# Kernel optimization log

Measured on AMD Instinct MI355X. Metric: run time of the kernel, lower is better.

## Reference

```python
import jax, jax.numpy as jnp
import numpy as np

ODIM = 8192      # output dim (slice target)
MSIZE = 64       # tile size
N_BLOCKS = 1024  # size of shared block bank


def setup_inputs() -> dict:
    key = jax.random.key(0)
    k1, k2, k3, k4 = jax.random.split(key, 4)
    x = jax.random.normal(k1, (256, 8192), dtype=jnp.float32)
    # bank of msize x msize module blocks (scaled like fan-in init)
    blocks = jax.random.normal(k2, (N_BLOCKS, MSIZE, MSIZE), dtype=jnp.float32) * 0.02
    bound = 1.0 / np.sqrt(ODIM).astype(np.float32)
    bias = jax.random.uniform(k3, (ODIM,), dtype=jnp.float32, minval=-bound, maxval=bound)
    # parts: [icount, ocount] indices into the block bank
    parts = jax.random.randint(k4, (128, 128), 0, N_BLOCKS)
    return {"x": x, "blocks": blocks, "bias": bias, "parts": parts}


def reference(x, blocks, bias, parts):
    icount, ocount = parts.shape
    m = blocks.shape[-1]
    # build_mosaic: gather blocks per parts and tile into a dense weight matrix
    fc = blocks[parts]                                   # [ic, oc, m, m]
    fc_mat = fc.transpose(0, 2, 1, 3).reshape(icount * m, ocount * m)
    # idim (8192) is divisible by msize, so pad is identity (rem == 0 branch)
    y = x @ fc_mat                                       # [B, oc*m]
    y = y[..., :ODIM] + bias                             # slice + bias; post = Identity
    return y
```

## Files before the change

kernel.cpp:

```cpp
#include <hip/hip_runtime.h>
#include <stdint.h>

#define BATCH 256
#define IDIM  8192
#define ODIM  8192
#define MS    64
#define IC    128
#define OC    128
#define NB    1024

#define BM 256
#define BN 256
#define BK 64
#define KSPLIT 8
#define KT (IC / KSPLIT)

#define ABUF(s) ((s) * 16384)
#define BBUF(s) (32768 + (s) * 16384)

typedef __bf16 bf16x8 __attribute__((ext_vector_type(8)));
typedef float  floatx4 __attribute__((ext_vector_type(4)));

#define WAITCNT_VM(n) ((((n) & 15) | (((n) >> 4) << 14)) | 0x70 | 0xF00)

__device__ __forceinline__ void async_load16(unsigned short* lds_p, const unsigned short* g_p) {
    __builtin_amdgcn_global_load_lds(
        (const __attribute__((address_space(1))) unsigned int*)g_p,
        (__attribute__((address_space(3))) unsigned int*)lds_p,
        16, 0, 0);
}

__device__ __forceinline__ unsigned short f32_to_bf16(float f) {
    unsigned int u = __float_as_uint(f);
    u += 0x7FFFu + ((u >> 16) & 1u);
    return (unsigned short)(u >> 16);
}

#define XCONV_BLKS 1024
#define PT_BLKS 64
__global__ void k_convert(const float* __restrict__ x, const float* __restrict__ blocks,
                          const int* __restrict__ parts,
                          unsigned short* __restrict__ xb, unsigned short* __restrict__ bt,
                          int* __restrict__ pT) {
    __shared__ float tile[MS][MS + 1];
    int b = blockIdx.x;
    if (b < NB) {
        const float4* src4 = (const float4*)(blocks + (size_t)b * MS * MS);
        unsigned short* dst = bt + (size_t)b * MS * MS;
        #pragma unroll
        for (int i = 0; i < 4; ++i) {
            int slot = i * 256 + threadIdx.x;
            int r = slot >> 4, c4 = (slot & 15) * 4;
            float4 v = src4[slot];
            tile[r][c4 + 0] = v.x; tile[r][c4 + 1] = v.y;
            tile[r][c4 + 2] = v.z; tile[r][c4 + 3] = v.w;
        }
        __syncthreads();
        #pragma unroll
        for (int i = 0; i < 2; ++i) {
            int slot = i * 256 + threadIdx.x;
            int c = slot >> 3, o = slot & 7;
            union { unsigned short s[8]; uint4 v; } u;
            #pragma unroll
            for (int j = 0; j < 8; ++j) u.s[j] = f32_to_bf16(tile[o * 8 + j][c]);
            *(uint4*)(dst + c * MS + o * 8) = u.v;
        }
    } else if (b < NB + XCONV_BLKS) {
        int t = (b - NB) * 256 + threadIdx.x;
        const float4* x4 = (const float4*)x;
        float4 a = x4[2 * t], bb = x4[2 * t + 1];
        union { unsigned short s[8]; uint4 v; } u;
        u.s[0] = f32_to_bf16(a.x);  u.s[1] = f32_to_bf16(a.y);
        u.s[2] = f32_to_bf16(a.z);  u.s[3] = f32_to_bf16(a.w);
        u.s[4] = f32_to_bf16(bb.x); u.s[5] = f32_to_bf16(bb.y);
        u.s[6] = f32_to_bf16(bb.z); u.s[7] = f32_to_bf16(bb.w);
        ((uint4*)xb)[t] = u.v;
    } else {
        int t = (b - NB - XCONV_BLKS) * 256 + threadIdx.x;
        int oc = t >> 7, ic = t & 127;
        pT[t] = parts[ic * OC + oc];
    }
}

extern __shared__ unsigned short smem[];

__global__ __launch_bounds__(512, 2)
void k_mosaic_gemm(const unsigned short* __restrict__ xb,
                   const unsigned short* __restrict__ bt,
                   const int* __restrict__ pT,
                   float* __restrict__ partial) {
    const int tid  = threadIdx.x;
    const int lane = tid & 63;
    const int wave = tid >> 6;
    const int wrow = wave >> 2;
    const int wcol = wave & 3;
    const int ks = blockIdx.x;
    const int nt = blockIdx.y;

    const int ob0 = nt * 4;
    const int kb0 = ks * KT;

    const int row  = lane & 15;
    const int quad = lane >> 4;

    int pv = pT[(ob0 + quad) * IC + kb0 + row];

    const int swz0 = ((quad)     ^ (row & 7)) << 3;
    const int swz1 = ((quad + 4) ^ (row & 7)) << 3;
    const int a_b0 = (wrow * 128 + row) * MS + swz0;
    const int a_b1 = (wrow * 128 + row) * MS + swz1;
    const int b_b0 = (wcol * 64 + row) * MS + swz0;
    const int b_b1 = (wcol * 64 + row) * MS + swz1;

    floatx4 acc[8][4];
    #pragma unroll
    for (int mi = 0; mi < 8; ++mi)
        #pragma unroll
        for (int ni = 0; ni < 4; ++ni)
            acc[mi][ni] = (floatx4){0.f, 0.f, 0.f, 0.f};

    bf16x8 af[4], bfr[4];

#define STAGE_A(dstS, kb) do {                                                \
    _Pragma("unroll")                                                         \
    for (int j = 0; j < 4; ++j) {                                             \
        int slot = j * 512 + tid;               \
        int m = slot >> 3;                                                    \
        int oct = (slot & 7) ^ (m & 7);                                       \
        async_load16(smem + ABUF(dstS) + slot * 8,                            \
                     xb + (size_t)m * IDIM + (kb) * MS + oct * 8);            \
    } } while (0)

#define STAGE_B(dstS, t) do {                                                 \
    _Pragma("unroll")                                                         \
    for (int j = 0; j < 4; ++j) {                                             \
        int q = __shfl(pv, j * 16 + (t));                                     \
        int slot = j * 512 + tid;                                             \
        int n = slot >> 3;                                                    \
        int oct = (slot & 7) ^ (n & 7);                                       \
        async_load16(smem + BBUF(dstS) + slot * 8,                            \
                     bt + (size_t)q * (MS * MS) + (n & 63) * MS + oct * 8);   \
    } } while (0)

#define BARRIER_PIN() do {                                                    \
    __builtin_amdgcn_sched_barrier(0);                                        \
    __builtin_amdgcn_s_barrier();                                             \
    __builtin_amdgcn_sched_barrier(0); } while (0)

#define LOAD_A(S, abase, mh) do {                                             \
    _Pragma("unroll")                                                         \
    for (int mi = 0; mi < 4; ++mi)                                            \
        af[mi] = *(const bf16x8*)(smem + ABUF(S) + (abase) + (mh) * 4096 + mi * 1024); \
    } while (0)

#define LOAD_B(S, bbase) do {                                                 \
    _Pragma("unroll")                                                         \
    for (int ni = 0; ni < 4; ++ni)                                            \
        bfr[ni] = *(const bf16x8*)(smem + BBUF(S) + (bbase) + ni * 1024);     \
    } while (0)

#define MFMA16(mh) do {                                                       \
    __builtin_amdgcn_s_setprio(1);                                            \
    _Pragma("unroll")                                                         \
    for (int mi = 0; mi < 4; ++mi)                                            \
        _Pragma("unroll")                                                     \
        for (int ni = 0; ni < 4; ++ni)                                        \
            acc[(mh) * 4 + mi][ni] = __builtin_amdgcn_mfma_f32_16x16x32_bf16( \
                af[mi], bfr[ni], acc[(mh) * 4 + mi][ni], 0, 0, 0);            \
    __builtin_amdgcn_s_setprio(0); } while (0)

#define TILE(t, curS, nxtS, DO_STAGE) do {                                    \
                                         \
    LOAD_A(curS, a_b0, 0); LOAD_B(curS, b_b0);                                \
    if (DO_STAGE) STAGE_A(nxtS, kb0 + (t) + 1);                               \
    BARRIER_PIN();                                                            \
    MFMA16(0);                                                                \
    BARRIER_PIN();                                                            \
                                         \
    LOAD_A(curS, a_b0, 1);                                                    \
    if (DO_STAGE) STAGE_B(nxtS, (t) + 1);                                     \
    BARRIER_PIN();                                                            \
    MFMA16(1);                                                                \
    BARRIER_PIN();                                                            \
                                                        \
    LOAD_A(curS, a_b1, 0); LOAD_B(curS, b_b1);                                \
    BARRIER_PIN();                                                            \
    MFMA16(0);                                                                \
    BARRIER_PIN();                                                            \
                  \
    LOAD_A(curS, a_b1, 1);                                                    \
    BARRIER_PIN();                                                            \
    MFMA16(1);                                                                \
    __builtin_amdgcn_sched_barrier(0);                                        \
    __builtin_amdgcn_s_waitcnt(WAITCNT_VM(0));                                \
    __builtin_amdgcn_s_barrier();                                             \
    __builtin_amdgcn_sched_barrier(0);                                        \
    } while (0)

    STAGE_A(0, kb0);
    STAGE_B(0, 0);
    __builtin_amdgcn_sched_barrier(0);
    __builtin_amdgcn_s_waitcnt(WAITCNT_VM(0));
    __builtin_amdgcn_s_barrier();
    __builtin_amdgcn_sched_barrier(0);

    #pragma unroll 1
    for (int t2 = 0; t2 < 14; t2 += 2) {
        TILE(t2,     0, 1, 1);
        TILE(t2 + 1, 1, 0, 1);
    }
    TILE(14, 0, 1, 1);
    TILE(15, 1, 0, 0);

    float* out = partial + (size_t)ks * ((size_t)BATCH * ODIM);
    #pragma unroll
    for (int mi8 = 0; mi8 < 8; ++mi8)
        #pragma unroll
        for (int ni = 0; ni < 4; ++ni)
            #pragma unroll
            for (int r = 0; r < 4; ++r) {
                int rowg = wrow * 128 + mi8 * 16 + quad * 4 + r;
                int colg = nt * BN + wcol * 64 + ni * 16 + row;
                out[(size_t)rowg * ODIM + colg] = acc[mi8][ni][r];
            }
}

__global__ void k_reduce_bias(const float* __restrict__ partial,
                              const float* __restrict__ bias,
                              float* __restrict__ out) {
    int t = blockIdx.x * 256 + threadIdx.x;
    const float4* b4 = (const float4*)bias;
    float4 c = b4[t & (ODIM / 4 - 1)];
    float4 r = {c.x, c.y, c.z, c.w};
    #pragma unroll
    for (int k = 0; k < KSPLIT; ++k) {
        const float4* p = (const float4*)(partial + (size_t)k * BATCH * ODIM);
        float4 a = p[t];
        r.x += a.x; r.y += a.y; r.z += a.z; r.w += a.w;
    }
    ((float4*)out)[t] = r;
}

extern "C" void kernel_launch(void* const* d_in, const int* in_sizes, int n_in,
                              void* d_out, int out_size, void* d_ws, size_t ws_size,
                              hipStream_t stream) {
    const float* x      = (const float*)d_in[0];
    const float* blocks = (const float*)d_in[1];
    const float* bias   = (const float*)d_in[2];
    const int*   parts  = (const int*)d_in[3];
    float* out = (float*)d_out;

    char* ws = (char*)d_ws;
    unsigned short* xb      = (unsigned short*)ws;
    unsigned short* btb     = (unsigned short*)(ws + (4u << 20));
    int*            pTr     = (int*)(ws + (12u << 20));
    float*          partial = (float*)(ws + (13u << 20));

    static bool attr_set = false;
    if (!attr_set) {
        hipFuncSetAttribute((const void*)k_mosaic_gemm,
                            hipFuncAttributeMaxDynamicSharedMemorySize, 128 * 1024);
        attr_set = true;
    }

    k_convert<<<NB + XCONV_BLKS + PT_BLKS, 256, 0, stream>>>(x, blocks, parts, xb, btb, pTr);
    k_mosaic_gemm<<<dim3(KSPLIT, ODIM / BN), 512, 128 * 1024, stream>>>(xb, btb, pTr, partial);
    k_reduce_bias<<<(BATCH * ODIM) / (256 * 4), 256, 0, stream>>>(partial, bias, out);
}
```

Baseline: 127.8 us.

## Triple-buffer B tiles and prefetch two stages ahead with partial waitcnt

```diff
diff --git a/kernel.cpp b/kernel.cpp
--- a/kernel.cpp
+++ b/kernel.cpp
@@ -131,10 +131,10 @@
                      xb + (size_t)m * IDIM + (kb) * MS + oct * 8);            \
     } } while (0)
 
-#define STAGE_B(dstS, t) do {                                                 \
+#define STAGE_B(dstS, tt) do {                                                \
     _Pragma("unroll")                                                         \
     for (int j = 0; j < 4; ++j) {                                             \
-        int q = __shfl(pv, j * 16 + (t));                                     \
+        int q = __shfl(pv, j * 16 + (tt));                                    \
         int slot = j * 512 + tid;                                             \
         int n = slot >> 3;                                                    \
         int oct = (slot & 7) ^ (n & 7);                                       \
@@ -169,48 +169,55 @@
                 af[mi], bfr[ni], acc[(mh) * 4 + mi][ni], 0, 0, 0);            \
     __builtin_amdgcn_s_setprio(0); } while (0)
 
-#define TILE(t, curS, nxtS, DO_STAGE) do {                                    \
-                                         \
-    LOAD_A(curS, a_b0, 0); LOAD_B(curS, b_b0);                                \
-    if (DO_STAGE) STAGE_A(nxtS, kb0 + (t) + 1);                               \
+#define TILE(t, AS, BS, AN, BN2, STA, STB, WN) do {                           \
+                                      \
+    LOAD_A(AS, a_b0, 0); LOAD_B(BS, b_b0);                                    \
+    if (STA) STAGE_A(AN, kb0 + (t) + 1);                                      \
     BARRIER_PIN();                                                            \
     MFMA16(0);                                                                \
     BARRIER_PIN();                                                            \
-                                         \
-    LOAD_A(curS, a_b0, 1);                                                    \
-    if (DO_STAGE) STAGE_B(nxtS, (t) + 1);                                     \
+                                      \
+    LOAD_A(AS, a_b0, 1);                                                      \
+    if (STB) STAGE_B(BN2, (t) + 2);                                           \
     BARRIER_PIN();                                                            \
     MFMA16(1);                                                                \
     BARRIER_PIN();                                                            \
                                                         \
-    LOAD_A(curS, a_b1, 0); LOAD_B(curS, b_b1);                                \
+    LOAD_A(AS, a_b1, 0); LOAD_B(BS, b_b1);                                    \
     BARRIER_PIN();                                                            \
     MFMA16(0);                                                                \
     BARRIER_PIN();                                                            \
-                  \
-    LOAD_A(curS, a_b1, 1);                                                    \
+             \
+    LOAD_A(AS, a_b1, 1);                                                      \
     BARRIER_PIN();                                                            \
     MFMA16(1);                                                                \
     __builtin_amdgcn_sched_barrier(0);                                        \
-    __builtin_amdgcn_s_waitcnt(WAITCNT_VM(0));                                \
+    if ((WN) >= 0) __builtin_amdgcn_s_waitcnt(WAITCNT_VM((WN) & 63));         \
     __builtin_amdgcn_s_barrier();                                             \
     __builtin_amdgcn_sched_barrier(0);                                        \
     } while (0)
 
     STAGE_A(0, kb0);
     STAGE_B(0, 0);
+    STAGE_B(1, 1);
     __builtin_amdgcn_sched_barrier(0);
-    __builtin_amdgcn_s_waitcnt(WAITCNT_VM(0));
+    __builtin_amdgcn_s_waitcnt(WAITCNT_VM(4));
     __builtin_amdgcn_s_barrier();
     __builtin_amdgcn_sched_barrier(0);
 
     #pragma unroll 1
-    for (int t2 = 0; t2 < 14; t2 += 2) {
-        TILE(t2,     0, 1, 1);
-        TILE(t2 + 1, 1, 0, 1);
-    }
-    TILE(14, 0, 1, 1);
-    TILE(15, 1, 0, 0);
+    for (int t6 = 0; t6 < 12; t6 += 6) {
+        TILE(t6 + 0, 0, 0, 1, 2, 1, 1, 4);
+        TILE(t6 + 1, 1, 1, 0, 0, 1, 1, 4);
+        TILE(t6 + 2, 0, 2, 1, 1, 1, 1, 4);
+        TILE(t6 + 3, 1, 0, 0, 2, 1, 1, 4);
+        TILE(t6 + 4, 0, 1, 1, 0, 1, 1, 4);
+        TILE(t6 + 5, 1, 2, 0, 1, 1, 1, 4);
+    }
+    TILE(12, 0, 0, 1, 2, 1, 1, 4);
+    TILE(13, 1, 1, 0, 0, 1, 1, 4);
+    TILE(14, 0, 2, 1, 0, 1, 0, 0);
+    TILE(15, 1, 0, 0, 0, 0, 0, -1);
 
     float* out = partial + (size_t)ks * ((size_t)BATCH * ODIM);
     #pragma unroll
@@ -259,11 +266,11 @@
     static bool attr_set = false;
     if (!attr_set) {
         hipFuncSetAttribute((const void*)k_mosaic_gemm,
-                            hipFuncAttributeMaxDynamicSharedMemorySize, 128 * 1024);
+                            hipFuncAttributeMaxDynamicSharedMemorySize, 160 * 1024);
         attr_set = true;
     }
 
     k_convert<<<NB + XCONV_BLKS + PT_BLKS, 256, 0, stream>>>(x, blocks, parts, xb, btb, pTr);
-    k_mosaic_gemm<<<dim3(KSPLIT, ODIM / BN), 512, 128 * 1024, stream>>>(xb, btb, pTr, partial);
+    k_mosaic_gemm<<<dim3(KSPLIT, ODIM / BN), 512, 160 * 1024, stream>>>(xb, btb, pTr, partial);
     k_reduce_bias<<<(BATCH * ODIM) / (256 * 4), 256, 0, stream>>>(partial, bias, out);
 }
```

Measured after the change: 128.0 us. No clear change (+0.1%).
